# Performance work log

Measured on AMD Instinct MI355X. Metric: run time of the kernel, lower is better.

Reference implementation:

```python
import jax, jax.numpy as jnp
import numpy as np

NUM_HEADS = 8

def setup_inputs() -> dict:
    key = jax.random.key(0)
    k1, k2, k3, k4, k5 = jax.random.split(key, 5)
    B, N, C = 4, 2048, 512
    x = jax.random.normal(k1, (B, N, C), dtype=jnp.float32)
    s = 1.0 / np.sqrt(C)
    qkv_w = jax.random.uniform(k2, (3 * C, C), dtype=jnp.float32, minval=-s, maxval=s)
    qkv_b = jax.random.uniform(k3, (3 * C,), dtype=jnp.float32, minval=-s, maxval=s)
    proj_w = jax.random.uniform(k4, (C, C), dtype=jnp.float32, minval=-s, maxval=s)
    proj_b = jax.random.uniform(k5, (C,), dtype=jnp.float32, minval=-s, maxval=s)
    return {"x": x, "qkv_w": qkv_w, "qkv_b": qkv_b, "proj_w": proj_w, "proj_b": proj_b}

def reference(x, qkv_w, qkv_b, proj_w, proj_b):
    B, N, C = x.shape
    H = NUM_HEADS
    D = C // H
    scale = D ** -0.5
    # qkv: [B,N,3C] -> [3,B,H,N,D]
    qkv = (jnp.einsum('bnc,oc->bno', x, qkv_w) + qkv_b)
    qkv = qkv.reshape(B, N, 3, H, D).transpose(2, 0, 3, 1, 4)
    q, k, v = qkv[0], qkv[1], qkv[2]
    attn = jnp.einsum('bhnd,bhmd->bhnm', q, k) * scale  # [B,H,N,N]
    attn = jax.nn.softmax(attn, axis=-1)
    out = jnp.einsum('bhnm,bhmd->bhnd', attn, v)  # [B,H,N,D]
    out = out.transpose(0, 2, 1, 3).reshape(B, N, C)
    return jnp.einsum('bnc,oc->bno', out, proj_w) + proj_b
```

## Files before the change

### kernel.cpp

```cpp
#include <hip/hip_runtime.h>
#include <stdint.h>


typedef short bf16x8 __attribute__((ext_vector_type(8)));
typedef float f32x2  __attribute__((ext_vector_type(2)));
typedef float f32x4  __attribute__((ext_vector_type(4)));
typedef float f32x16 __attribute__((ext_vector_type(16)));
typedef unsigned int u32x4 __attribute__((ext_vector_type(4)));

__device__ __forceinline__ unsigned short f2bf(float f) {
    unsigned int u = __builtin_bit_cast(unsigned int, f);
    u += 0x7fffu + ((u >> 16) & 1u);
    return (unsigned short)(u >> 16);
}
__device__ __forceinline__ unsigned int pk2(float a, float b) {
    return (unsigned int)f2bf(a) | ((unsigned int)f2bf(b) << 16);
}
__device__ __forceinline__ float fexp2(float x) {
    return __builtin_amdgcn_exp2f(x);
}
__device__ __forceinline__ bf16x8 ld8_f32(const float* __restrict__ p) {
    float4 f0 = *(const float4*)p;
    float4 f1 = *(const float4*)(p + 4);
    u32x4 u = {pk2(f0.x, f0.y), pk2(f0.z, f0.w), pk2(f1.x, f1.y), pk2(f1.z, f1.w)};
    return __builtin_bit_cast(bf16x8, u);
}
__device__ __forceinline__ void async16(const void* g, void* l) {
    __builtin_amdgcn_global_load_lds(
        (const __attribute__((address_space(1))) unsigned int*)g,
        (__attribute__((address_space(3))) unsigned int*)l,
        16, 0, 0);
}

#define MFMA16(a, b, c) __builtin_amdgcn_mfma_f32_16x16x32_bf16((a), (b), (c), 0, 0, 0)
#define MFMA32(a, b, c) __builtin_amdgcn_mfma_f32_32x32x16_bf16((a), (b), (c), 0, 0, 0)

__global__ void cvt_bf16(const float* __restrict__ x,
                         const float* __restrict__ w,
                         const float* __restrict__ w2,
                         unsigned short* __restrict__ xb,
                         unsigned short* __restrict__ wb,
                         unsigned short* __restrict__ wb2)
{
    const int G = 524288 + 98304 + 32768;
    for (int idx = blockIdx.x * 256 + threadIdx.x; idx < G; idx += gridDim.x * 256) {
        if (idx < 524288)
            *(bf16x8*)(xb + (size_t)idx * 8) = ld8_f32(x + (size_t)idx * 8);
        else if (idx < 524288 + 98304) {
            int j = idx - 524288;
            *(bf16x8*)(wb + (size_t)j * 8) = ld8_f32(w + (size_t)j * 8);
        } else {
            int j = idx - 524288 - 98304;
            *(bf16x8*)(wb2 + (size_t)j * 8) = ld8_f32(w2 + (size_t)j * 8);
        }
    }
}

__global__ __launch_bounds__(256, 4)
void gemm_qkv(const unsigned short* __restrict__ A,
              const unsigned short* __restrict__ B,
              const float* __restrict__ bias,
              unsigned short* __restrict__ out0,
              unsigned short* __restrict__ out1,
              unsigned short* __restrict__ out2,
              int K)
{
    __shared__ unsigned short sA[128 * 32];
    __shared__ unsigned short sB[128 * 32];

    const int tid  = threadIdx.x;
    const int wave = tid >> 6, lane = tid & 63;
    const int l = lane & 15, q16 = lane >> 4;
    const int wm = wave >> 1, wn = wave & 1;
    const int bid = blockIdx.x;
    const int slot = bid >> 3;
    const int m0 = ((bid & 7) * 8 + slot / 12) * 128;
    const int n0 = (slot % 12) * 128;

    f32x4 acc[4][4];
#pragma unroll
    for (int i = 0; i < 4; ++i)
#pragma unroll
        for (int j = 0; j < 4; ++j)
            acc[i][j] = (f32x4){0.f, 0.f, 0.f, 0.f};

    for (int k0 = 0; k0 < K; k0 += 32) {
#pragma unroll
        for (int call = 0; call < 2; ++call) {
            int L = call * 256 + tid;
            int r = L >> 2, c = L & 3;
            async16(A + (size_t)(m0 + r) * K + k0 + c * 8, sA + L * 8);
            async16(B + (size_t)(n0 + r) * K + k0 + c * 8, sB + L * 8);
        }
        __syncthreads();

        bf16x8 af[4], bfr[4];
#pragma unroll
        for (int i = 0; i < 4; ++i)
            af[i] = *(const bf16x8*)(sA + ((wm * 64 + i * 16 + l) * 4 + q16) * 8);
#pragma unroll
        for (int j = 0; j < 4; ++j)
            bfr[j] = *(const bf16x8*)(sB + ((wn * 64 + j * 16 + l) * 4 + q16) * 8);
#pragma unroll
        for (int i = 0; i < 4; ++i)
#pragma unroll
            for (int j = 0; j < 4; ++j)
                acc[i][j] = MFMA16(af[i], bfr[j], acc[i][j]);
        __syncthreads();
    }

    const float lscale = 0.18033688f;
#pragma unroll
    for (int i = 0; i < 4; ++i) {
#pragma unroll
        for (int j = 0; j < 4; ++j) {
            int col = n0 + wn * 64 + j * 16 + l;
            float bv = bias[col];
#pragma unroll
            for (int r = 0; r < 4; ++r) {
                int row = m0 + wm * 64 + i * 16 + q16 * 4 + r;
                float val = acc[i][j][r] + bv;
                int which = col >> 9;
                int h = (col >> 6) & 7, d = col & 63;
                int b = row >> 11, n = row & 2047;
                if (which == 0)
                    out0[(size_t)(((b * 8 + h) * 2048) + n) * 64 + d] = f2bf(val * lscale);
                else if (which == 1)
                    out1[(size_t)(((b * 8 + h) * 2048) + n) * 64 + d] = f2bf(val);
                else {
                    int np = (n & ~12) | ((n & 8) >> 1) | ((n & 4) << 1);
                    out2[(size_t)(((b * 8 + h) * 64) + d) * 2048 + np] = f2bf(val);
                }
            }
        }
    }
}

__global__ __launch_bounds__(256, 4)
void gemm_out(const unsigned short* __restrict__ A,
              const unsigned short* __restrict__ B,
              const float* __restrict__ bias,
              float* __restrict__ outf,
              int K, int N)
{
    __shared__ unsigned short sA[64 * 32];
    __shared__ unsigned short sB[128 * 32];

    const int tid  = threadIdx.x;
    const int wave = tid >> 6, lane = tid & 63;
    const int l = lane & 15, q16 = lane >> 4;
    const int wm = wave >> 1, wn = wave & 1;
    const int bid = blockIdx.x;
    const int slot = bid >> 3;
    const int m0 = ((bid & 7) * 16 + (slot >> 2)) * 64;
    const int n0 = (slot & 3) * 128;

    f32x4 acc[2][4];
#pragma unroll
    for (int i = 0; i < 2; ++i)
#pragma unroll
        for (int j = 0; j < 4; ++j)
            acc[i][j] = (f32x4){0.f, 0.f, 0.f, 0.f};

    for (int k0 = 0; k0 < K; k0 += 32) {
        {
            int r = tid >> 2, c = tid & 3;
            async16(A + (size_t)(m0 + r) * K + k0 + c * 8, sA + tid * 8);
        }
#pragma unroll
        for (int call = 0; call < 2; ++call) {
            int L = call * 256 + tid;
            int r = L >> 2, c = L & 3;
            async16(B + (size_t)(n0 + r) * K + k0 + c * 8, sB + L * 8);
        }
        __syncthreads();

        bf16x8 af[2], bfr[4];
#pragma unroll
        for (int i = 0; i < 2; ++i)
            af[i] = *(const bf16x8*)(sA + ((wm * 32 + i * 16 + l) * 4 + q16) * 8);
#pragma unroll
        for (int j = 0; j < 4; ++j)
            bfr[j] = *(const bf16x8*)(sB + ((wn * 64 + j * 16 + l) * 4 + q16) * 8);
#pragma unroll
        for (int i = 0; i < 2; ++i)
#pragma unroll
            for (int j = 0; j < 4; ++j)
                acc[i][j] = MFMA16(af[i], bfr[j], acc[i][j]);
        __syncthreads();
    }

#pragma unroll
    for (int i = 0; i < 2; ++i) {
#pragma unroll
        for (int j = 0; j < 4; ++j) {
            int col = n0 + wn * 64 + j * 16 + l;
            float bv = bias[col];
#pragma unroll
            for (int r = 0; r < 4; ++r) {
                int row = m0 + wm * 32 + i * 16 + q16 * 4 + r;
                outf[(size_t)row * N + col] = acc[i][j][r] + bv;
            }
        }
    }
}

__global__ __launch_bounds__(512, 4)
void attn_fused(const unsigned short* __restrict__ Q,
                const unsigned short* __restrict__ Km,
                const unsigned short* __restrict__ Vt,
                unsigned short* __restrict__ O)
{
    __shared__ unsigned short sAll[32768];

    const int tid  = threadIdx.x;
    const int wave = tid >> 6, lane = tid & 63;
    const int l31 = lane & 31, h = lane >> 5;
    const int swz = l31 & 7;
    const int qq = wave >> 1, kh = wave & 1;
    const int bid = blockIdx.x;
    const int slot = bid >> 3;
    const int bh = (bid & 7) * 4 + (slot >> 4);
    const int n0 = (slot & 15) * 128;
    const int q0 = n0 + qq * 32;

    const unsigned short* Kp = Km + (size_t)bh * 2048 * 64;
    const unsigned short* Vp = Vt + (size_t)bh * 64 * 2048;
    unsigned short* sKf = sAll;
    unsigned short* sVf = sAll + 16384;

    int ka[4], va[2][2];
#pragma unroll
    for (int ks = 0; ks < 4; ++ks)
        ka[ks] = (kh * 64 + l31) * 64 + ((ks * 2 + h) ^ swz) * 8;
#pragma unroll
    for (int m1 = 0; m1 < 2; ++m1)
#pragma unroll
        for (int ks2 = 0; ks2 < 2; ++ks2)
            va[m1][ks2] = l31 * 128 + ((m1 * 4 + ks2 * 2 + h) ^ swz) * 8 + kh * 64;

    int ksrc[2], vsrc[2], dstv[2];
#pragma unroll
    for (int c = 0; c < 2; ++c) {
        int s = c * 512 + tid;
        int rk = s >> 3;
        ksrc[c] = rk * 64 + ((s & 7) ^ (rk & 7)) * 8;
        int rv = s >> 4;
        vsrc[c] = rv * 2048 + ((s & 15) ^ (rv & 7)) * 8;
        dstv[c] = s * 8;
    }

    bf16x8 qf[4];
#pragma unroll
    for (int ks = 0; ks < 4; ++ks)
        qf[ks] = *(const bf16x8*)(Q + (size_t)(bh * 2048 + q0 + l31) * 64
                                  + ks * 16 + h * 8);

    f32x16 oacc[2];
#pragma unroll
    for (int dt = 0; dt < 2; ++dt)
#pragma unroll
        for (int e = 0; e < 16; ++e) oacc[dt][e] = 0.f;
    f32x16 Zv;
#pragma unroll
    for (int e = 0; e < 16; ++e) Zv[e] = 0.f;
    f32x2 l2 = {0.f, 0.f};

#pragma unroll
    for (int c = 0; c < 2; ++c) {
        async16(Kp + ksrc[c], (void*)(sKf + dstv[c]));
        async16(Vp + vsrc[c], (void*)(sVf + dstv[c]));
    }
    __syncthreads();

    for (int it = 0; it < 16; ++it) {
        const int nb = ((it + 1) & 1) * 8192;
        if (it < 15) {
            int kv = (it + 1) * 128;
#pragma unroll
            for (int c = 0; c < 2; ++c)
                async16(Kp + (size_t)kv * 64 + ksrc[c], (void*)(sKf + nb + dstv[c]));
        }

        f32x16 sacc[2];
#pragma unroll
        for (int mt = 0; mt < 2; ++mt) {
            bf16x8 kf0 = *(const bf16x8*)(sKf + ka[0] + mt * 2048);
            sacc[mt] = MFMA32(kf0, qf[0], Zv);
#pragma unroll
            for (int ks = 1; ks < 4; ++ks) {
                bf16x8 kf = *(const bf16x8*)(sKf + ka[ks] + mt * 2048);
                sacc[mt] = MFMA32(kf, qf[ks], sacc[mt]);
            }
        }

        if (it < 15) {
            int kv = (it + 1) * 128;
#pragma unroll
            for (int c = 0; c < 2; ++c)
                async16(Vp + (size_t)kv + vsrc[c], (void*)(sVf + nb + dstv[c]));
        }

#pragma unroll
        for (int mt = 0; mt < 2; ++mt) {
            unsigned int pk[4][2];
#pragma unroll
            for (int g = 0; g < 4; ++g) {
                float p0 = fexp2(sacc[mt][4 * g + 0]);
                float p1 = fexp2(sacc[mt][4 * g + 1]);
                float p2 = fexp2(sacc[mt][4 * g + 2]);
                float p3 = fexp2(sacc[mt][4 * g + 3]);
                l2 += (f32x2){p0, p1};
                l2 += (f32x2){p2, p3};
                pk[g][0] = __builtin_amdgcn_perm(
                    __builtin_bit_cast(unsigned int, p1),
                    __builtin_bit_cast(unsigned int, p0), 0x07060302u);
                pk[g][1] = __builtin_amdgcn_perm(
                    __builtin_bit_cast(unsigned int, p3),
                    __builtin_bit_cast(unsigned int, p2), 0x07060302u);
            }
#pragma unroll
            for (int ks2 = 0; ks2 < 2; ++ks2) {
                u32x4 bu;
                bu[0] = pk[2 * ks2][0];
                bu[1] = pk[2 * ks2][1];
                bu[2] = pk[2 * ks2 + 1][0];
                bu[3] = pk[2 * ks2 + 1][1];
                bf16x8 bfrag = __builtin_bit_cast(bf16x8, bu);
#pragma unroll
                for (int dt = 0; dt < 2; ++dt) {
                    bf16x8 vf = *(const bf16x8*)(sVf + va[mt][ks2] + dt * 4096);
                    oacc[dt] = MFMA32(vf, bfrag, oacc[dt]);
                }
            }
        }

#pragma unroll
        for (int ks = 0; ks < 4; ++ks) ka[ks] ^= 8192;
        va[0][0] ^= 8192; va[0][1] ^= 8192; va[1][0] ^= 8192; va[1][1] ^= 8192;
        __syncthreads();
    }

    float* sf = (float*)sAll;
    float* sl = sf + 8192;
    if (kh == 1) {
        const int base = qq * 2048 + lane * 32;
#pragma unroll
        for (int dt = 0; dt < 2; ++dt) {
            int chunk = dt ^ (lane & 1);
            *(f32x16*)(sf + base + chunk * 16) = oacc[dt];
        }
        *(f32x2*)(sl + qq * 128 + lane * 2) = l2;
    }
    __syncthreads();
    if (kh == 0) {
        const int base = qq * 2048 + lane * 32;
#pragma unroll
        for (int dt = 0; dt < 2; ++dt) {
            int chunk = dt ^ (lane & 1);
            f32x16 part = *(const f32x16*)(sf + base + chunk * 16);
#pragma unroll
            for (int e = 0; e < 16; ++e) oacc[dt][e] += part[e];
        }
        l2 += *(const f32x2*)(sl + qq * 128 + lane * 2);

        float l_run = l2[0] + l2[1];
        l_run += __shfl_xor(l_run, 32);
        float inv = 1.f / fmaxf(l_run, 1e-20f);
        const int b = bh >> 3, hh = bh & 7;
        unsigned short* obase = O + ((size_t)(b * 2048 + q0 + l31)) * 512 + hh * 64;
#pragma unroll
        for (int dt = 0; dt < 2; ++dt)
#pragma unroll
            for (int g = 0; g < 4; ++g) {
                int d = dt * 32 + 8 * g + 4 * h;
                unsigned int w0 = pk2(oacc[dt][4 * g + 0] * inv,
                                      oacc[dt][4 * g + 1] * inv);
                unsigned int w1 = pk2(oacc[dt][4 * g + 2] * inv,
                                      oacc[dt][4 * g + 3] * inv);
                uint2 w = {w0, w1};
                *(uint2*)(obase + d) = w;
            }
    }
}

extern "C" void kernel_launch(void* const* d_in, const int* in_sizes, int n_in,
                              void* d_out, int out_size, void* d_ws, size_t ws_size,
                              hipStream_t stream)
{
    const float* x      = (const float*)d_in[0];
    const float* qkv_w  = (const float*)d_in[1];
    const float* qkv_b  = (const float*)d_in[2];
    const float* proj_w = (const float*)d_in[3];
    const float* proj_b = (const float*)d_in[4];

    const size_t PER = 4u * 8u * 2048u * 64u;
    unsigned short* q_ws  = (unsigned short*)d_ws;
    unsigned short* k_ws  = q_ws  + PER;
    unsigned short* vt_ws = k_ws  + PER;
    unsigned short* ao_ws = vt_ws + PER;
    unsigned short* wb2   = ao_ws + PER;

    unsigned short* xb = (unsigned short*)d_out;
    unsigned short* wb = xb + PER;

    cvt_bf16<<<dim3(640), 256, 0, stream>>>(x, qkv_w, proj_w, xb, wb, wb2);
    gemm_qkv<<<dim3(768), 256, 0, stream>>>(xb, wb, qkv_b, q_ws, k_ws, vt_ws, 512);
    attn_fused<<<dim3(512), 512, 0, stream>>>(q_ws, k_ws, vt_ws, ao_ws);
    gemm_out<<<dim3(512), 256, 0, stream>>>(ao_ws, wb2, proj_b, (float*)d_out, 512, 512);
}
```

Before: 158.6 us.

## Triple-buffer K/V with two-tile prefetch and double attention block size

```diff
diff --git a/kernel.cpp b/kernel.cpp
--- a/kernel.cpp
+++ b/kernel.cpp
@@ -205,13 +205,13 @@
     }
 }
 
-__global__ __launch_bounds__(512, 4)
+__global__ __launch_bounds__(1024, 4)
 void attn_fused(const unsigned short* __restrict__ Q,
                 const unsigned short* __restrict__ Km,
                 const unsigned short* __restrict__ Vt,
                 unsigned short* __restrict__ O)
 {
-    __shared__ unsigned short sAll[32768];
+    __shared__ unsigned short sAll[49152];
 
     const int tid  = threadIdx.x;
     const int wave = tid >> 6, lane = tid & 63;
@@ -220,14 +220,14 @@
     const int qq = wave >> 1, kh = wave & 1;
     const int bid = blockIdx.x;
     const int slot = bid >> 3;
-    const int bh = (bid & 7) * 4 + (slot >> 4);
-    const int n0 = (slot & 15) * 128;
-    const int q0 = n0 + qq * 32;
+    const int bh = (bid & 7) * 4 + (slot >> 3);
+    const int qc = slot & 7;
+    const int q0 = qc * 256 + qq * 32;
 
     const unsigned short* Kp = Km + (size_t)bh * 2048 * 64;
     const unsigned short* Vp = Vt + (size_t)bh * 64 * 2048;
     unsigned short* sKf = sAll;
-    unsigned short* sVf = sAll + 16384;
+    unsigned short* sVf = sAll + 24576;
 
     int ka[4], va[2][2];
 #pragma unroll
@@ -239,16 +239,12 @@
         for (int ks2 = 0; ks2 < 2; ++ks2)
             va[m1][ks2] = l31 * 128 + ((m1 * 4 + ks2 * 2 + h) ^ swz) * 8 + kh * 64;
 
-    int ksrc[2], vsrc[2], dstv[2];
-#pragma unroll
-    for (int c = 0; c < 2; ++c) {
-        int s = c * 512 + tid;
-        int rk = s >> 3;
-        ksrc[c] = rk * 64 + ((s & 7) ^ (rk & 7)) * 8;
-        int rv = s >> 4;
-        vsrc[c] = rv * 2048 + ((s & 15) ^ (rv & 7)) * 8;
-        dstv[c] = s * 8;
-    }
+    const int s = tid;
+    const int rk = s >> 3;
+    const int ksrc = rk * 64 + ((s & 7) ^ (rk & 7)) * 8;
+    const int rv = s >> 4;
+    const int vsrc = rv * 2048 + ((s & 15) ^ (rv & 7)) * 8;
+    const int dsl = s * 8;
 
     bf16x8 qf[4];
 #pragma unroll
@@ -266,39 +262,42 @@
     for (int e = 0; e < 16; ++e) Zv[e] = 0.f;
     f32x2 l2 = {0.f, 0.f};
 
-#pragma unroll
-    for (int c = 0; c < 2; ++c) {
-        async16(Kp + ksrc[c], (void*)(sKf + dstv[c]));
-        async16(Vp + vsrc[c], (void*)(sVf + dstv[c]));
-    }
-    __syncthreads();
+    async16(Kp + ksrc, (void*)(sKf + dsl));
+    async16(Vp + vsrc, (void*)(sVf + dsl));
+    async16(Kp + (size_t)128 * 64 + ksrc, (void*)(sKf + 8192 + dsl));
+    async16(Vp + (size_t)128 + vsrc, (void*)(sVf + 8192 + dsl));
+    asm volatile("s_waitcnt vmcnt(2)" ::: "memory");
+    __builtin_amdgcn_s_barrier();
+    __builtin_amdgcn_sched_barrier(0);
+
+    int off0 = 0, off1 = 8192, off2 = 16384;
 
     for (int it = 0; it < 16; ++it) {
-        const int nb = ((it + 1) & 1) * 8192;
-        if (it < 15) {
-            int kv = (it + 1) * 128;
-#pragma unroll
-            for (int c = 0; c < 2; ++c)
-                async16(Kp + (size_t)kv * 64 + ksrc[c], (void*)(sKf + nb + dstv[c]));
-        }
-
+        if (it < 14) {
+            size_t kv = (size_t)(it + 2) * 128;
+            async16(Kp + kv * 64 + ksrc, (void*)(sKf + off2 + dsl));
+            async16(Vp + kv + vsrc, (void*)(sVf + off2 + dsl));
+        }
+
+        const unsigned short* sKc = sKf + off0;
+        const unsigned short* sVc = sVf + off0;
         f32x16 sacc[2];
-#pragma unroll
-        for (int mt = 0; mt < 2; ++mt) {
-            bf16x8 kf0 = *(const bf16x8*)(sKf + ka[0] + mt * 2048);
-            sacc[mt] = MFMA32(kf0, qf[0], Zv);
+        {
+            bf16x8 kf00 = *(const bf16x8*)(sKc + ka[0]);
+            bf16x8 kf01 = *(const bf16x8*)(sKc + ka[0] + 2048);
+            __builtin_amdgcn_s_setprio(1);
+            sacc[0] = MFMA32(kf00, qf[0], Zv);
+            sacc[1] = MFMA32(kf01, qf[0], Zv);
+            __builtin_amdgcn_s_setprio(0);
 #pragma unroll
             for (int ks = 1; ks < 4; ++ks) {
-                bf16x8 kf = *(const bf16x8*)(sKf + ka[ks] + mt * 2048);
-                sacc[mt] = MFMA32(kf, qf[ks], sacc[mt]);
-            }
-        }
-
-        if (it < 15) {
-            int kv = (it + 1) * 128;
-#pragma unroll
-            for (int c = 0; c < 2; ++c)
-                async16(Vp + (size_t)kv + vsrc[c], (void*)(sVf + nb + dstv[c]));
+                bf16x8 kf0 = *(const bf16x8*)(sKc + ka[ks]);
+                bf16x8 kf1 = *(const bf16x8*)(sKc + ka[ks] + 2048);
+                __builtin_amdgcn_s_setprio(1);
+                sacc[0] = MFMA32(kf0, qf[ks], sacc[0]);
+                sacc[1] = MFMA32(kf1, qf[ks], sacc[1]);
+                __builtin_amdgcn_s_setprio(0);
+            }
         }
 
 #pragma unroll
@@ -329,20 +328,31 @@
                 bf16x8 bfrag = __builtin_bit_cast(bf16x8, bu);
 #pragma unroll
                 for (int dt = 0; dt < 2; ++dt) {
-                    bf16x8 vf = *(const bf16x8*)(sVf + va[mt][ks2] + dt * 4096);
+                    bf16x8 vf = *(const bf16x8*)(sVc + va[mt][ks2] + dt * 4096);
+                    __builtin_amdgcn_s_setprio(1);
                     oacc[dt] = MFMA32(vf, bfrag, oacc[dt]);
+                    __builtin_amdgcn_s_setprio(0);
                 }
             }
         }
 
-#pragma unroll
-        for (int ks = 0; ks < 4; ++ks) ka[ks] ^= 8192;
-        va[0][0] ^= 8192; va[0][1] ^= 8192; va[1][0] ^= 8192; va[1][1] ^= 8192;
-        __syncthreads();
-    }
-
+        if (it < 14) {
+            asm volatile("s_waitcnt vmcnt(2)" ::: "memory");
+        } else if (it == 14) {
+            asm volatile("s_waitcnt vmcnt(0)" ::: "memory");
+        }
+        if (it < 15) {
+            asm volatile("s_waitcnt lgkmcnt(0)" ::: "memory");
+            __builtin_amdgcn_s_barrier();
+            __builtin_amdgcn_sched_barrier(0);
+        }
+
+        int t = off0; off0 = off1; off1 = off2; off2 = t;
+    }
+
+    __syncthreads();
     float* sf = (float*)sAll;
-    float* sl = sf + 8192;
+    float* sl = sf + 16384;
     if (kh == 1) {
         const int base = qq * 2048 + lane * 32;
 #pragma unroll
@@ -406,6 +416,6 @@
 
     cvt_bf16<<<dim3(640), 256, 0, stream>>>(x, qkv_w, proj_w, xb, wb, wb2);
     gemm_qkv<<<dim3(768), 256, 0, stream>>>(xb, wb, qkv_b, q_ws, k_ws, vt_ws, 512);
-    attn_fused<<<dim3(512), 512, 0, stream>>>(q_ws, k_ws, vt_ws, ao_ws);
+    attn_fused<<<dim3(256), 1024, 0, stream>>>(q_ws, k_ws, vt_ws, ao_ws);
     gemm_out<<<dim3(512), 256, 0, stream>>>(ao_ws, wb2, proj_b, (float*)d_out, 512, 512);
 }
```

Result: no change. 155.8 us (-1.7%).

## Pre-swizzle K and V into MFMA fragment layout and load directly from global

Applied to the files above, without the earlier changes.

```diff
diff --git a/kernel.cpp b/kernel.cpp
--- a/kernel.cpp
+++ b/kernel.cpp
@@ -121,15 +121,26 @@
                 int row = m0 + wm * 64 + i * 16 + q16 * 4 + r;
                 float val = acc[i][j][r] + bv;
                 int which = col >> 9;
-                int h = (col >> 6) & 7, d = col & 63;
+                int hd = (col >> 6) & 7, d = col & 63;
                 int b = row >> 11, n = row & 2047;
-                if (which == 0)
-                    out0[(size_t)(((b * 8 + h) * 2048) + n) * 64 + d] = f2bf(val * lscale);
-                else if (which == 1)
-                    out1[(size_t)(((b * 8 + h) * 2048) + n) * 64 + d] = f2bf(val);
-                else {
+                int bh = b * 8 + hd;
+                if (which == 0) {
+                    out0[(size_t)((bh * 2048) + n) * 64 + d] = f2bf(val * lscale);
+                } else if (which == 1) {
+                    int t = n >> 7, kh2 = (n >> 6) & 1, mt = (n >> 5) & 1;
+                    int l31o = n & 31;
+                    int ks = (d >> 4) & 3, h2 = (d >> 3) & 1, e = d & 7;
+                    size_t frag = ((((size_t)bh * 16 + t) * 2 + kh2) * 2 + mt) * 4 + ks;
+                    out1[frag * 512 + (h2 * 32 + l31o) * 8 + e] = f2bf(val);
+                } else {
                     int np = (n & ~12) | ((n & 8) >> 1) | ((n & 4) << 1);
-                    out2[(size_t)(((b * 8 + h) * 64) + d) * 2048 + np] = f2bf(val);
+                    int t = np >> 7, kh2 = (np >> 6) & 1;
+                    int c = (np >> 3) & 7, e = np & 7;
+                    int m1 = (c >> 2) & 1, ks2 = (c >> 1) & 1, h2 = c & 1;
+                    int dt = d >> 5, l31o = d & 31;
+                    size_t frag = (((((size_t)bh * 16 + t) * 2 + kh2) * 2 + m1) * 2
+                                   + ks2) * 2 + dt;
+                    out2[frag * 512 + (h2 * 32 + l31o) * 8 + e] = f2bf(val);
                 }
             }
         }
@@ -205,50 +216,26 @@
     }
 }
 
-__global__ __launch_bounds__(512, 4)
+__global__ __launch_bounds__(512, 3)
 void attn_fused(const unsigned short* __restrict__ Q,
-                const unsigned short* __restrict__ Km,
-                const unsigned short* __restrict__ Vt,
+                const unsigned short* __restrict__ Kfr,
+                const unsigned short* __restrict__ Vfr,
                 unsigned short* __restrict__ O)
 {
-    __shared__ unsigned short sAll[32768];
+    __shared__ float smrg[8192 + 512];
 
     const int tid  = threadIdx.x;
     const int wave = tid >> 6, lane = tid & 63;
     const int l31 = lane & 31, h = lane >> 5;
-    const int swz = l31 & 7;
-    const int qq = wave >> 1, kh = wave & 1;
+    const int qq = wave & 3, kh = wave >> 2;
     const int bid = blockIdx.x;
     const int slot = bid >> 3;
     const int bh = (bid & 7) * 4 + (slot >> 4);
-    const int n0 = (slot & 15) * 128;
-    const int q0 = n0 + qq * 32;
-
-    const unsigned short* Kp = Km + (size_t)bh * 2048 * 64;
-    const unsigned short* Vp = Vt + (size_t)bh * 64 * 2048;
-    unsigned short* sKf = sAll;
-    unsigned short* sVf = sAll + 16384;
-
-    int ka[4], va[2][2];
-#pragma unroll
-    for (int ks = 0; ks < 4; ++ks)
-        ka[ks] = (kh * 64 + l31) * 64 + ((ks * 2 + h) ^ swz) * 8;
-#pragma unroll
-    for (int m1 = 0; m1 < 2; ++m1)
-#pragma unroll
-        for (int ks2 = 0; ks2 < 2; ++ks2)
-            va[m1][ks2] = l31 * 128 + ((m1 * 4 + ks2 * 2 + h) ^ swz) * 8 + kh * 64;
-
-    int ksrc[2], vsrc[2], dstv[2];
-#pragma unroll
-    for (int c = 0; c < 2; ++c) {
-        int s = c * 512 + tid;
-        int rk = s >> 3;
-        ksrc[c] = rk * 64 + ((s & 7) ^ (rk & 7)) * 8;
-        int rv = s >> 4;
-        vsrc[c] = rv * 2048 + ((s & 15) ^ (rv & 7)) * 8;
-        dstv[c] = s * 8;
-    }
+    const int qc = slot & 15;
+    const int q0 = qc * 128 + qq * 32;
+
+    const unsigned short* Kb = Kfr + (size_t)bh * 131072 + kh * 4096 + lane * 8;
+    const unsigned short* Vb = Vfr + (size_t)bh * 131072 + kh * 4096 + lane * 8;
 
     bf16x8 qf[4];
 #pragma unroll
@@ -266,95 +253,75 @@
     for (int e = 0; e < 16; ++e) Zv[e] = 0.f;
     f32x2 l2 = {0.f, 0.f};
 
-#pragma unroll
-    for (int c = 0; c < 2; ++c) {
-        async16(Kp + ksrc[c], (void*)(sKf + dstv[c]));
-        async16(Vp + vsrc[c], (void*)(sVf + dstv[c]));
-    }
+    for (int t = 0; t < 16; ++t) {
+        const size_t tb = (size_t)t * 8192;
+#pragma unroll
+        for (int mt = 0; mt < 2; ++mt) {
+            const size_t sb = tb + (size_t)mt * 2048;
+
+            bf16x8 kA0 = *(const bf16x8*)(Kb + sb + 0 * 512);
+            bf16x8 kA1 = *(const bf16x8*)(Kb + sb + 1 * 512);
+            bf16x8 kA2 = *(const bf16x8*)(Kb + sb + 2 * 512);
+            bf16x8 kA3 = *(const bf16x8*)(Kb + sb + 3 * 512);
+            bf16x8 v00 = *(const bf16x8*)(Vb + sb + 0 * 1024 + 0 * 512);
+            bf16x8 v01 = *(const bf16x8*)(Vb + sb + 0 * 1024 + 1 * 512);
+            bf16x8 v10 = *(const bf16x8*)(Vb + sb + 1 * 1024 + 0 * 512);
+            bf16x8 v11 = *(const bf16x8*)(Vb + sb + 1 * 1024 + 1 * 512);
+
+            f32x16 s0;
+            __builtin_amdgcn_s_setprio(1);
+            s0 = MFMA32(kA0, qf[0], Zv);
+            s0 = MFMA32(kA1, qf[1], s0);
+            s0 = MFMA32(kA2, qf[2], s0);
+            s0 = MFMA32(kA3, qf[3], s0);
+            __builtin_amdgcn_s_setprio(0);
+
+            unsigned int pk0[4][2];
+#pragma unroll
+            for (int g = 0; g < 4; ++g) {
+                float a0 = fexp2(s0[4 * g + 0]);
+                float a1 = fexp2(s0[4 * g + 1]);
+                float a2 = fexp2(s0[4 * g + 2]);
+                float a3 = fexp2(s0[4 * g + 3]);
+                l2 += (f32x2){a0, a1};
+                l2 += (f32x2){a2, a3};
+                pk0[g][0] = __builtin_amdgcn_perm(
+                    __builtin_bit_cast(unsigned int, a1),
+                    __builtin_bit_cast(unsigned int, a0), 0x07060302u);
+                pk0[g][1] = __builtin_amdgcn_perm(
+                    __builtin_bit_cast(unsigned int, a3),
+                    __builtin_bit_cast(unsigned int, a2), 0x07060302u);
+            }
+            u32x4 bu;
+            bu[0] = pk0[0][0]; bu[1] = pk0[0][1]; bu[2] = pk0[1][0]; bu[3] = pk0[1][1];
+            bf16x8 f0 = __builtin_bit_cast(bf16x8, bu);
+            bu[0] = pk0[2][0]; bu[1] = pk0[2][1]; bu[2] = pk0[3][0]; bu[3] = pk0[3][1];
+            bf16x8 f1 = __builtin_bit_cast(bf16x8, bu);
+
+            __builtin_amdgcn_s_setprio(1);
+            oacc[0] = MFMA32(v00, f0, oacc[0]);
+            oacc[1] = MFMA32(v01, f0, oacc[1]);
+            oacc[0] = MFMA32(v10, f1, oacc[0]);
+            oacc[1] = MFMA32(v11, f1, oacc[1]);
+            __builtin_amdgcn_s_setprio(0);
+        }
+    }
+
     __syncthreads();
-
-    for (int it = 0; it < 16; ++it) {
-        const int nb = ((it + 1) & 1) * 8192;
-        if (it < 15) {
-            int kv = (it + 1) * 128;
-#pragma unroll
-            for (int c = 0; c < 2; ++c)
-                async16(Kp + (size_t)kv * 64 + ksrc[c], (void*)(sKf + nb + dstv[c]));
-        }
-
-        f32x16 sacc[2];
-#pragma unroll
-        for (int mt = 0; mt < 2; ++mt) {
-            bf16x8 kf0 = *(const bf16x8*)(sKf + ka[0] + mt * 2048);
-            sacc[mt] = MFMA32(kf0, qf[0], Zv);
-#pragma unroll
-            for (int ks = 1; ks < 4; ++ks) {
-                bf16x8 kf = *(const bf16x8*)(sKf + ka[ks] + mt * 2048);
-                sacc[mt] = MFMA32(kf, qf[ks], sacc[mt]);
-            }
-        }
-
-        if (it < 15) {
-            int kv = (it + 1) * 128;
-#pragma unroll
-            for (int c = 0; c < 2; ++c)
-                async16(Vp + (size_t)kv + vsrc[c], (void*)(sVf + nb + dstv[c]));
-        }
-
-#pragma unroll
-        for (int mt = 0; mt < 2; ++mt) {
-            unsigned int pk[4][2];
-#pragma unroll
-            for (int g = 0; g < 4; ++g) {
-                float p0 = fexp2(sacc[mt][4 * g + 0]);
-                float p1 = fexp2(sacc[mt][4 * g + 1]);
-                float p2 = fexp2(sacc[mt][4 * g + 2]);
-                float p3 = fexp2(sacc[mt][4 * g + 3]);
-                l2 += (f32x2){p0, p1};
-                l2 += (f32x2){p2, p3};
-                pk[g][0] = __builtin_amdgcn_perm(
-                    __builtin_bit_cast(unsigned int, p1),
-                    __builtin_bit_cast(unsigned int, p0), 0x07060302u);
-                pk[g][1] = __builtin_amdgcn_perm(
-                    __builtin_bit_cast(unsigned int, p3),
-                    __builtin_bit_cast(unsigned int, p2), 0x07060302u);
-            }
-#pragma unroll
-            for (int ks2 = 0; ks2 < 2; ++ks2) {
-                u32x4 bu;
-                bu[0] = pk[2 * ks2][0];
-                bu[1] = pk[2 * ks2][1];
-                bu[2] = pk[2 * ks2 + 1][0];
-                bu[3] = pk[2 * ks2 + 1][1];
-                bf16x8 bfrag = __builtin_bit_cast(bf16x8, bu);
-#pragma unroll
-                for (int dt = 0; dt < 2; ++dt) {
-                    bf16x8 vf = *(const bf16x8*)(sVf + va[mt][ks2] + dt * 4096);
-                    oacc[dt] = MFMA32(vf, bfrag, oacc[dt]);
-                }
-            }
-        }
-
-#pragma unroll
-        for (int ks = 0; ks < 4; ++ks) ka[ks] ^= 8192;
-        va[0][0] ^= 8192; va[0][1] ^= 8192; va[1][0] ^= 8192; va[1][1] ^= 8192;
-        __syncthreads();
-    }
-
-    float* sf = (float*)sAll;
-    float* sl = sf + 8192;
+    float* sf = smrg;
+    float* sl = smrg + 8192;
     if (kh == 1) {
-        const int base = qq * 2048 + lane * 32;
+        const int base = (qq * 64 + lane) * 32;
 #pragma unroll
         for (int dt = 0; dt < 2; ++dt) {
             int chunk = dt ^ (lane & 1);
             *(f32x16*)(sf + base + chunk * 16) = oacc[dt];
         }
-        *(f32x2*)(sl + qq * 128 + lane * 2) = l2;
+        *(f32x2*)(sl + (qq * 64 + lane) * 2) = l2;
     }
     __syncthreads();
     if (kh == 0) {
-        const int base = qq * 2048 + lane * 32;
+        const int base = (qq * 64 + lane) * 32;
 #pragma unroll
         for (int dt = 0; dt < 2; ++dt) {
             int chunk = dt ^ (lane & 1);
@@ -362,7 +329,7 @@
 #pragma unroll
             for (int e = 0; e < 16; ++e) oacc[dt][e] += part[e];
         }
-        l2 += *(const f32x2*)(sl + qq * 128 + lane * 2);
+        l2 += *(const f32x2*)(sl + (qq * 64 + lane) * 2);
 
         float l_run = l2[0] + l2[1];
         l_run += __shfl_xor(l_run, 32);
```

New measurement: 157.4 us. Within noise of the previous version (-0.7%).
